# Performance work log

Measured on AMD Instinct MI355X. Metric: run time of the kernel, lower is better.

The kernel has to match this reference:

```python
import jax, jax.numpy as jnp
import numpy as np

N, C_IN, EDGE = 32, 64, 64
C_OUT, KH, KW = 128, 3, 3
STRIDE, PAD = 1, 1


def setup_inputs() -> dict:
    key = jax.random.key(0)
    k1, k2, k3 = jax.random.split(key, 3)
    s = 2.4 / (C_IN * KW * KH)  # lecun_init bound from the module
    x = jax.random.normal(k1, (N, C_IN, EDGE, EDGE), dtype=jnp.float32)
    weight = jax.random.uniform(k2, (C_IN * KW * KH, C_OUT), dtype=jnp.float32, minval=-s, maxval=s)
    bias = jax.random.uniform(k3, (1, C_OUT, 1, 1), dtype=jnp.float32, minval=-s, maxval=s)
    return {"input": x, "weight": weight, "bias": bias}


def reference(input, weight, bias):
    # torch.nn.Unfold orders the patch axis as c*kh*kw + i*kw + j, so the
    # (C_in*kh*kw, C_out) weight reshapes to (C_in, kh, kw, C_out).
    k = weight.reshape(C_IN, KH, KW, C_OUT)
    k = jnp.transpose(k, (3, 0, 1, 2))  # OIHW
    out = jax.lax.conv_general_dilated(
        input, k,
        window_strides=(STRIDE, STRIDE),
        padding=[(PAD, PAD), (PAD, PAD)],
        dimension_numbers=("NCHW", "OIHW", "NCHW"),
    )
    return out + bias
```

## Files before the change

kernel.cpp:

```cpp
#include <hip/hip_runtime.h>
#include <cstdint>
#include <cstddef>

#define CIN   64
#define CH_   64
#define CW_   64
#define COUT  128

typedef short  s16x8  __attribute__((ext_vector_type(8)));
typedef float  f32x16 __attribute__((ext_vector_type(16)));

__device__ __forceinline__ unsigned short f32_to_bf16(float f) {
    unsigned int u = __builtin_bit_cast(unsigned int, f);
    u = u + 0x7FFFu + ((u >> 16) & 1u);
    return (unsigned short)(u >> 16);
}

#define GLD_LDS16(g, l) __builtin_amdgcn_global_load_lds(                      \
    (const __attribute__((address_space(1))) void*)(g),                        \
    (__attribute__((address_space(3))) void*)(l), 16, 0, 0)

__global__ void wconv_prep(const float* __restrict__ wgt, unsigned short* __restrict__ wdst) {
    int tid = blockIdx.x * 256 + threadIdx.x;
    if (tid >= 9 * 128 * 64) return;
    int tap = tid >> 13;
    int rem = tid & 8191;
    int co  = rem >> 6;
    int c   = rem & 63;
    float f = wgt[(c * 9 + tap) * COUT + co];
    int off = tap * 16384 + co * 128 + ((((c >> 3) ^ (co & 7))) << 4) + (c & 7) * 2;
    wdst[off >> 1] = f32_to_bf16(f);
}

__global__ __launch_bounds__(256, 2) void conv_mfma(
    const float* __restrict__ x,
    const float* __restrict__ bias,
    const unsigned short* __restrict__ wbf,
    float* __restrict__ out)
{
    __shared__ __align__(16) unsigned char lds_x[4 * 66 * 128];
    __shared__ __align__(16) unsigned char lds_w[2][128 * 128];

    const int tid  = threadIdx.x;
    const int lane = tid & 63;
    const int wid  = tid >> 6;
    const int hi   = lane >> 5;
    const int l31  = lane & 31;
    const int wm   = wid >> 1;
    const int wn   = wid & 1;
    const int hb   = blockIdx.x;
    const int n    = blockIdx.y;
    const int h0   = hb * 2;

    const char* wsrc = (const char*)wbf;
    const int   boff = wid * 4096;

    #pragma unroll
    for (int k = 0; k < 4; ++k)
        GLD_LDS16(wsrc + boff + k * 1024 + lane * 16, &lds_w[0][boff + k * 1024]);

    {
        const float* xn = x + (size_t)n * CIN * CH_ * CW_;
        for (int idx = tid; idx < 4 * 8 * 66; idx += 256) {
            int col = idx % 66;
            int rh  = idx / 66;
            int ck  = rh & 7;
            int r   = rh >> 3;
            int grow = h0 - 1 + r;
            int gcol = col - 1;
            bool v = (grow >= 0) && (grow < CH_) && (gcol >= 0) && (gcol < CW_);
            s16x8 pk;
            #pragma unroll
            for (int e = 0; e < 8; ++e) {
                float f = v ? xn[((size_t)(ck * 8 + e) * CH_ + grow) * CW_ + gcol] : 0.0f;
                pk[e] = (short)f32_to_bf16(f);
            }
            int off = (r * 66 + col) * 128 + ((ck ^ (col & 7)) << 4);
            *(s16x8*)(lds_x + off) = pk;
        }
    }
    __syncthreads();

    f32x16 acc00 = {}, acc01 = {}, acc10 = {}, acc11 = {};

    const int          coB  = wn * 64 + l31;
    const unsigned int bOff = (unsigned)coB * 128;
    const int          xorB = l31 & 7;

    #pragma unroll
    for (int tap = 0; tap < 9; ++tap) {
        const int cur = tap & 1;
        if (tap < 8) {
            #pragma unroll
            for (int k = 0; k < 4; ++k)
                GLD_LDS16(wsrc + (tap + 1) * 16384 + boff + k * 1024 + lane * 16,
                          &lds_w[cur ^ 1][boff + k * 1024]);
            asm volatile("s_waitcnt vmcnt(4)" ::: "memory");
        } else {
            asm volatile("s_waitcnt vmcnt(0)" ::: "memory");
        }
        __builtin_amdgcn_s_barrier();

        const int i = tap / 3, j = tap % 3;
        const int r    = wm + i;
        const int colj = l31 + j;
        const unsigned int aBase = (unsigned)(r * 66 + colj) * 128;
        const int          xorA  = colj & 7;

        #pragma unroll
        for (int cc = 0; cc < 4; ++cc) {
            const int ch = cc * 2 + hi;
            const unsigned int aO0 = aBase + (unsigned)((ch ^ xorA) << 4);
            const unsigned int aO1 = aO0 + 32 * 128;
            const unsigned int bO0 = bOff + (unsigned)((ch ^ xorB) << 4);
            const unsigned int bO1 = bO0 + 32 * 128;
            s16x8 a0 = *(const s16x8*)(lds_x + aO0);
            s16x8 a1 = *(const s16x8*)(lds_x + aO1);
            s16x8 b0 = *(const s16x8*)(lds_w[cur] + bO0);
            s16x8 b1 = *(const s16x8*)(lds_w[cur] + bO1);
            acc00 = __builtin_amdgcn_mfma_f32_32x32x16_bf16(a0, b0, acc00, 0, 0, 0);
            acc01 = __builtin_amdgcn_mfma_f32_32x32x16_bf16(a0, b1, acc01, 0, 0, 0);
            acc10 = __builtin_amdgcn_mfma_f32_32x32x16_bf16(a1, b0, acc10, 0, 0, 0);
            acc11 = __builtin_amdgcn_mfma_f32_32x32x16_bf16(a1, b1, acc11, 0, 0, 0);
        }
        __builtin_amdgcn_s_barrier();
    }

    const int h = h0 + wm;
    #pragma unroll
    for (int fn = 0; fn < 2; ++fn) {
        const int co = wn * 64 + fn * 32 + l31;
        const float bv = bias[co];
        float* op = out + (((size_t)n * COUT + co) * CH_ + h) * CW_ + 4 * hi;
        #pragma unroll
        for (int fm = 0; fm < 2; ++fm) {
            const f32x16 a = fn == 0 ? (fm == 0 ? acc00 : acc10)
                                     : (fm == 0 ? acc01 : acc11);
            #pragma unroll
            for (int q = 0; q < 4; ++q) {
                float4 v = make_float4(a[4*q+0] + bv, a[4*q+1] + bv,
                                       a[4*q+2] + bv, a[4*q+3] + bv);
                *(float4*)(op + fm * 32 + 8 * q) = v;
            }
        }
    }
}

__global__ __launch_bounds__(256) void conv_direct_f32(
    const float* __restrict__ x, const float* __restrict__ wgt,
    const float* __restrict__ bias, float* __restrict__ out)
{
    const int w = threadIdx.x, ty = threadIdx.y;
    const int cog = blockIdx.x, h = blockIdx.y, n = blockIdx.z;
    const int co0 = cog * 32 + ty * 8;
    float acc[8];
    #pragma unroll
    for (int k = 0; k < 8; ++k) acc[k] = bias[co0 + k];
    const float* xn = x + (size_t)n * CIN * CH_ * CW_;
    for (int c = 0; c < CIN; ++c) {
        const float* xc = xn + (size_t)c * CH_ * CW_;
        #pragma unroll
        for (int i = 0; i < 3; ++i) {
            const int hh = h - 1 + i;
            if (hh < 0 || hh >= CH_) continue;
            const float* xr = xc + hh * CW_;
            #pragma unroll
            for (int j = 0; j < 3; ++j) {
                const int ww = w - 1 + j;
                const float v = (ww >= 0 && ww < CW_) ? xr[ww] : 0.0f;
                const float* wp = wgt + (size_t)((c * 9 + i * 3 + j) * COUT) + co0;
                const float4 w0 = *reinterpret_cast<const float4*>(wp);
                const float4 w1 = *reinterpret_cast<const float4*>(wp + 4);
                acc[0] += v * w0.x; acc[1] += v * w0.y; acc[2] += v * w0.z; acc[3] += v * w0.w;
                acc[4] += v * w1.x; acc[5] += v * w1.y; acc[6] += v * w1.z; acc[7] += v * w1.w;
            }
        }
    }
    float* op = out + (((size_t)n * COUT + co0) * CH_ + h) * CW_ + w;
    #pragma unroll
    for (int k = 0; k < 8; ++k) op[(size_t)k * CH_ * CW_] = acc[k];
}

extern "C" void kernel_launch(void* const* d_in, const int* in_sizes, int n_in,
                              void* d_out, int out_size, void* d_ws, size_t ws_size,
                              hipStream_t stream) {
    const float* x    = (const float*)d_in[0];
    const float* wgt  = (const float*)d_in[1];
    const float* bias = (const float*)d_in[2];
    float* out        = (float*)d_out;

    if (ws_size >= 9 * 128 * 64 * sizeof(unsigned short)) {
        wconv_prep<<<288, 256, 0, stream>>>(wgt, (unsigned short*)d_ws);
        conv_mfma<<<dim3(32, 32), 256, 0, stream>>>(x, bias, (const unsigned short*)d_ws, out);
    } else {
        conv_direct_f32<<<dim3(4, 64, 32), dim3(64, 4, 1), 0, stream>>>(x, wgt, bias, out);
    }
}
```

Before: 121.1 us.

## Load conv weights directly to registers, vectorize input staging, swizzle block order

Drops the LDS double buffer for weights. Each wave now reads its B fragments straight from global memory into registers, using a new pre-tiled bf16 layout, and ping-pongs two register sets across the 9 taps, which removes the per-tap barriers. Input staging now uses float4 loads, with each thread writing four columns plus separate zero padding for the edges. Blocks are launched on a 1D grid with a swizzled (n, h) mapping, and the occupancy hint rises to 3 blocks. This costs more VGPRs for weight fragments and relies on L2/L1 hits for weight reloads.

```diff
diff --git a/kernel.cpp b/kernel.cpp
--- a/kernel.cpp
+++ b/kernel.cpp
@@ -16,30 +16,25 @@
     return (unsigned short)(u >> 16);
 }
 
-#define GLD_LDS16(g, l) __builtin_amdgcn_global_load_lds(                      \
-    (const __attribute__((address_space(1))) void*)(g),                        \
-    (__attribute__((address_space(3))) void*)(l), 16, 0, 0)
-
-__global__ void wconv_prep(const float* __restrict__ wgt, unsigned short* __restrict__ wdst) {
+__global__ __launch_bounds__(256) void wconv_prep(const float* __restrict__ wgt,
+                                                  unsigned short* __restrict__ wdst) {
     int tid = blockIdx.x * 256 + threadIdx.x;
-    if (tid >= 9 * 128 * 64) return;
-    int tap = tid >> 13;
-    int rem = tid & 8191;
-    int co  = rem >> 6;
-    int c   = rem & 63;
-    float f = wgt[(c * 9 + tap) * COUT + co];
-    int off = tap * 16384 + co * 128 + ((((c >> 3) ^ (co & 7))) << 4) + (c & 7) * 2;
-    wdst[off >> 1] = f32_to_bf16(f);
+    if (tid >= 576 * 128) return;
+    int row = tid >> 7;
+    int co  = tid & 127;
+    int c   = row / 9;
+    int tap = row - c * 9;
+    float f = wgt[tid];
+    wdst[((tap * 8 + (c >> 3)) * 128 + co) * 8 + (c & 7)] = f32_to_bf16(f);
 }
 
-__global__ __launch_bounds__(256, 2) void conv_mfma(
+__global__ __launch_bounds__(256, 3) void conv_mfma(
     const float* __restrict__ x,
     const float* __restrict__ bias,
     const unsigned short* __restrict__ wbf,
     float* __restrict__ out)
 {
     __shared__ __align__(16) unsigned char lds_x[4 * 66 * 128];
-    __shared__ __align__(16) unsigned char lds_w[2][128 * 128];
 
     const int tid  = threadIdx.x;
     const int lane = tid & 63;
@@ -48,83 +43,84 @@
     const int l31  = lane & 31;
     const int wm   = wid >> 1;
     const int wn   = wid & 1;
-    const int hb   = blockIdx.x;
-    const int n    = blockIdx.y;
-    const int h0   = hb * 2;
 
-    const char* wsrc = (const char*)wbf;
-    const int   boff = wid * 4096;
+    const int bid = blockIdx.x;
+    const int swz = (bid & 7) * 128 + (bid >> 3);
+    const int n   = swz >> 5;
+    const int hb  = swz & 31;
+    const int h0  = hb * 2;
+
+    const float* xn = x + (size_t)n * CIN * CH_ * CW_;
 
     #pragma unroll
-    for (int k = 0; k < 4; ++k)
-        GLD_LDS16(wsrc + boff + k * 1024 + lane * 16, &lds_w[0][boff + k * 1024]);
-
-    {
-        const float* xn = x + (size_t)n * CIN * CH_ * CW_;
-        for (int idx = tid; idx < 4 * 8 * 66; idx += 256) {
-            int col = idx % 66;
-            int rh  = idx / 66;
-            int ck  = rh & 7;
-            int r   = rh >> 3;
-            int grow = h0 - 1 + r;
-            int gcol = col - 1;
-            bool v = (grow >= 0) && (grow < CH_) && (gcol >= 0) && (gcol < CW_);
-            s16x8 pk;
+    for (int it = 0; it < 2; ++it) {
+        const int idx = tid + it * 256;
+        const int g  = idx & 15;
+        const int ck = (idx >> 4) & 7;
+        const int r  = idx >> 7;
+        const int grow = h0 - 1 + r;
+        s16x8 pk[4] = {};
+        if (grow >= 0 && grow < CH_) {
             #pragma unroll
             for (int e = 0; e < 8; ++e) {
-                float f = v ? xn[((size_t)(ck * 8 + e) * CH_ + grow) * CW_ + gcol] : 0.0f;
-                pk[e] = (short)f32_to_bf16(f);
+                const float4 v = *(const float4*)(xn + ((size_t)(ck * 8 + e) * CH_ + grow) * CW_ + 4 * g);
+                pk[0][e] = (short)f32_to_bf16(v.x);
+                pk[1][e] = (short)f32_to_bf16(v.y);
+                pk[2][e] = (short)f32_to_bf16(v.z);
+                pk[3][e] = (short)f32_to_bf16(v.w);
             }
-            int off = (r * 66 + col) * 128 + ((ck ^ (col & 7)) << 4);
-            *(s16x8*)(lds_x + off) = pk;
         }
+        #pragma unroll
+        for (int q = 0; q < 4; ++q) {
+            const int t = 4 * g + 1 + q;
+            *(s16x8*)(lds_x + (r * 66 + t) * 128 + ((ck ^ (t & 7)) << 4)) = pk[q];
+        }
+    }
+    if (tid < 64) {
+        const int t  = (tid & 1) ? 65 : 0;
+        const int ck = (tid >> 1) & 7;
+        const int r  = tid >> 4;
+        s16x8 z = {};
+        *(s16x8*)(lds_x + (r * 66 + t) * 128 + ((ck ^ (t & 7)) << 4)) = z;
     }
     __syncthreads();
 
     f32x16 acc00 = {}, acc01 = {}, acc10 = {}, acc11 = {};
+    const unsigned base0 = (unsigned)((wm * 66 + l31) * 128);
+    const s16x8* wB  = (const s16x8*)wbf;
+    const int bbase  = wn * 64 + l31 + hi * 128;
 
-    const int          coB  = wn * 64 + l31;
-    const unsigned int bOff = (unsigned)coB * 128;
-    const int          xorB = l31 & 7;
+#define LOADB(dst, tap) do {                                                   \
+    _Pragma("unroll") for (int cc = 0; cc < 4; ++cc) {                         \
+        dst[2*cc]   = wB[(tap) * 1024 + cc * 256 + bbase];                     \
+        dst[2*cc+1] = wB[(tap) * 1024 + cc * 256 + bbase + 32];                \
+    } } while (0)
 
+#define COMP(bb, tap) do {                                                     \
+    const int i_ = (tap) / 3, j_ = (tap) % 3;                                  \
+    const unsigned aBase = base0 + (unsigned)((i_ * 66 + j_) * 128);           \
+    const int xA = (l31 + j_) & 7;                                             \
+    _Pragma("unroll") for (int cc = 0; cc < 4; ++cc) {                         \
+        const int ch = cc * 2 + hi;                                            \
+        const unsigned aO0 = aBase + ((unsigned)(ch ^ xA) << 4);               \
+        s16x8 a0 = *(const s16x8*)(lds_x + aO0);                               \
+        s16x8 a1 = *(const s16x8*)(lds_x + aO0 + 32 * 128);                    \
+        acc00 = __builtin_amdgcn_mfma_f32_32x32x16_bf16(a0, bb[2*cc],   acc00, 0, 0, 0); \
+        acc01 = __builtin_amdgcn_mfma_f32_32x32x16_bf16(a0, bb[2*cc+1], acc01, 0, 0, 0); \
+        acc10 = __builtin_amdgcn_mfma_f32_32x32x16_bf16(a1, bb[2*cc],   acc10, 0, 0, 0); \
+        acc11 = __builtin_amdgcn_mfma_f32_32x32x16_bf16(a1, bb[2*cc+1], acc11, 0, 0, 0); \
+    } } while (0)
+
+    s16x8 bA[8], bB[8];
+    LOADB(bA, 0);
     #pragma unroll
-    for (int tap = 0; tap < 9; ++tap) {
-        const int cur = tap & 1;
-        if (tap < 8) {
-            #pragma unroll
-            for (int k = 0; k < 4; ++k)
-                GLD_LDS16(wsrc + (tap + 1) * 16384 + boff + k * 1024 + lane * 16,
-                          &lds_w[cur ^ 1][boff + k * 1024]);
-            asm volatile("s_waitcnt vmcnt(4)" ::: "memory");
-        } else {
-            asm volatile("s_waitcnt vmcnt(0)" ::: "memory");
-        }
-        __builtin_amdgcn_s_barrier();
-
-        const int i = tap / 3, j = tap % 3;
-        const int r    = wm + i;
-        const int colj = l31 + j;
-        const unsigned int aBase = (unsigned)(r * 66 + colj) * 128;
-        const int          xorA  = colj & 7;
-
-        #pragma unroll
-        for (int cc = 0; cc < 4; ++cc) {
-            const int ch = cc * 2 + hi;
-            const unsigned int aO0 = aBase + (unsigned)((ch ^ xorA) << 4);
-            const unsigned int aO1 = aO0 + 32 * 128;
-            const unsigned int bO0 = bOff + (unsigned)((ch ^ xorB) << 4);
-            const unsigned int bO1 = bO0 + 32 * 128;
-            s16x8 a0 = *(const s16x8*)(lds_x + aO0);
-            s16x8 a1 = *(const s16x8*)(lds_x + aO1);
-            s16x8 b0 = *(const s16x8*)(lds_w[cur] + bO0);
-            s16x8 b1 = *(const s16x8*)(lds_w[cur] + bO1);
-            acc00 = __builtin_amdgcn_mfma_f32_32x32x16_bf16(a0, b0, acc00, 0, 0, 0);
-            acc01 = __builtin_amdgcn_mfma_f32_32x32x16_bf16(a0, b1, acc01, 0, 0, 0);
-            acc10 = __builtin_amdgcn_mfma_f32_32x32x16_bf16(a1, b0, acc10, 0, 0, 0);
-            acc11 = __builtin_amdgcn_mfma_f32_32x32x16_bf16(a1, b1, acc11, 0, 0, 0);
-        }
-        __builtin_amdgcn_s_barrier();
+    for (int tt = 0; tt < 4; ++tt) {
+        LOADB(bB, 2 * tt + 1);
+        COMP(bA, 2 * tt);
+        LOADB(bA, 2 * tt + 2);
+        COMP(bB, 2 * tt + 1);
     }
+    COMP(bA, 8);
 
     const int h = h0 + wm;
     #pragma unroll
@@ -144,6 +140,8 @@
             }
         }
     }
+#undef LOADB
+#undef COMP
 }
 
 __global__ __launch_bounds__(256) void conv_direct_f32(
@@ -189,9 +187,9 @@
     const float* bias = (const float*)d_in[2];
     float* out        = (float*)d_out;
 
-    if (ws_size >= 9 * 128 * 64 * sizeof(unsigned short)) {
+    if (ws_size >= (size_t)(9 * 8 * 128 * 8) * sizeof(unsigned short)) {
         wconv_prep<<<288, 256, 0, stream>>>(wgt, (unsigned short*)d_ws);
-        conv_mfma<<<dim3(32, 32), 256, 0, stream>>>(x, bias, (const unsigned short*)d_ws, out);
+        conv_mfma<<<1024, 256, 0, stream>>>(x, bias, (const unsigned short*)d_ws, out);
     } else {
         conv_direct_f32<<<dim3(4, 64, 32), dim3(64, 4, 1), 0, stream>>>(x, wgt, bias, out);
     }
```

After: 114.1 us. -5.8%, faster.
